# Optimization experiments

Hardware: AMD Instinct MI355X
Metric: run time of the kernel (lower is better)

## Reference

```python
import jax, jax.numpy as jnp
import numpy as np

T, B, I, H, L, O = 512, 64, 128, 512, 2, 256


def _lstm_layer(x, Wih, Whh, b):
    """One LSTM layer over time. x:[T,B,in] -> (ys:[T,B,H], hT:[B,H], cT:[B,H]).
    PyTorch gate order: i, f, g, o. Zero initial state (module's zero buffers)."""
    Hs = Whh.shape[1]
    # Precompute input contribution for all timesteps (one big GEMM).
    xg = jnp.einsum('tbi,gi->tbg', x, Wih) + b  # [T,B,4H]

    def step(carry, xt):
        h, c = carry
        g = xt + h @ Whh.T  # [B,4H]
        i, f, gg, o = jnp.split(g, 4, axis=-1)
        c = jax.nn.sigmoid(f) * c + jax.nn.sigmoid(i) * jnp.tanh(gg)
        h = jax.nn.sigmoid(o) * jnp.tanh(c)
        return (h, c), h

    h0 = jnp.zeros((x.shape[1], Hs), x.dtype)
    (hT, cT), ys = jax.lax.scan(step, (h0, h0), xg)
    return ys, hT, cT


def setup_inputs() -> dict:
    key = jax.random.key(0)
    ks = jax.random.split(key, 9)
    s = 1.0 / np.sqrt(H)  # torch default uniform(-1/sqrt(H), 1/sqrt(H)) scale
    u = lambda k, shp: jax.random.uniform(k, shp, jnp.float32, -s, s)
    return {
        'x': jax.random.normal(ks[0], (T, B, I), jnp.float32),
        'W_ih0': u(ks[1], (4 * H, I)),
        'W_hh0': u(ks[2], (4 * H, H)),
        'b0': u(ks[3], (4 * H,)),  # b_ih + b_hh combined
        'W_ih1': u(ks[4], (4 * H, H)),
        'W_hh1': u(ks[5], (4 * H, H)),
        'b1': u(ks[6], (4 * H,)),
        'fc_w': u(ks[7], (O, H)),
        'fc_b': u(ks[8], (O,)),
    }


def reference(x, W_ih0, W_hh0, b0, W_ih1, W_hh1, b1, fc_w, fc_b):
    y0, h0, c0 = _lstm_layer(x, W_ih0, W_hh0, b0)
    y1, h1, c1 = _lstm_layer(y0, W_ih1, W_hh1, b1)
    fc = jnp.einsum('tbh,oh->tbo', y1, fc_w) + fc_b  # fused output projection
    hN = jnp.stack([h0, h1])  # [L,B,H]
    cN = jnp.stack([c0, c1])
    return fc, (hN, cN)
```

## Files before the change

kernel.cpp:

```cpp
#include <hip/hip_runtime.h>
#include <hip/hip_bf16.h>

#define T_SEQ 512
#define BATCH 64
#define IN0   128
#define HID   512
#define OUTF  256
#define G4    (4*HID)
#define NWG_L 64
#define FSTR  32

typedef __attribute__((ext_vector_type(8))) short short8;
typedef __attribute__((ext_vector_type(4))) float f32x4;
typedef unsigned short u16;
typedef unsigned long long u64;

__device__ __forceinline__ float sigmoidf_(float x) { return 1.f / (1.f + __expf(-x)); }
__device__ __forceinline__ float tanhf_(float x)    { return 1.f - 2.f / (1.f + __expf(2.f * x)); }

__device__ __forceinline__ u16 f2bf(float f) {
    union { float f; unsigned u; } a; a.f = f;
    unsigned u = a.u;
    return (u16)((u + 0x7fffu + ((u >> 16) & 1u)) >> 16);
}

__device__ __forceinline__ void wave_poll_ge(const unsigned* flags, int lane, unsigned tgt) {
    unsigned it = 0;
    for (;;) {
        unsigned v = __hip_atomic_load(flags + (size_t)lane * FSTR,
                                       __ATOMIC_RELAXED, __HIP_MEMORY_SCOPE_AGENT);
        if (__all((int)(v >= tgt))) return;
        __builtin_amdgcn_s_sleep(1);
        if ((++it & 2047u) == 0u)
            (void)__hip_atomic_load(flags, __ATOMIC_ACQUIRE, __HIP_MEMORY_SCOPE_AGENT);
    }
}

__global__ void cvt_f32_bf16(const float* __restrict__ in, u16* __restrict__ out, int n4) {
    int i = blockIdx.x * blockDim.x + threadIdx.x;
    if (i < n4) {
        float4 v = reinterpret_cast<const float4*>(in)[i];
        ushort4 o;
        o.x = f2bf(v.x); o.y = f2bf(v.y); o.z = f2bf(v.z); o.w = f2bf(v.w);
        reinterpret_cast<ushort4*>(out)[i] = o;
    }
}

template<int LAYER>
__device__ __forceinline__ void run_layer(
    const u16* __restrict__ asrc,
    const u16* __restrict__ wih, const u16* __restrict__ whh,
    const float* __restrict__ bias,
    u16* __restrict__ ybuf,
    float* __restrict__ hNout, float* __restrict__ cNout,
    unsigned* flags_own, unsigned* flags_dep, int g,
    u16 (*lds_w)[32][512], float (*lds_g)[33], float (*lds_b)[16],
    unsigned (*lds_h)[4])
{
    constexpr int KIN = (LAYER == 0) ? IN0 : HID;
    constexpr int KS1 = KIN / 32;
    constexpr int KS  = KS1 + 16;

    const int tid  = threadIdx.x;
    const int lane = tid & 63;
    const int w    = tid >> 6;
    const int ubase = 8 * g;

    for (int idx = tid; idx < 2 * KS * 64; idx += 256) {
        int nt  = (idx >= KS * 64) ? 1 : 0;
        int rem = idx - nt * KS * 64;
        int ks = rem >> 6, s = rem & 63, q = s & 15, kq = s >> 4;
        int r = (q >> 2) * HID + ubase + 4 * nt + (q & 3);
        const u16* src = (ks < KS1)
            ? wih + (size_t)r * KIN + (size_t)ks * 32 + kq * 8
            : whh + (size_t)r * HID + (size_t)(ks - KS1) * 32 + kq * 8;
        *reinterpret_cast<uint4*>(&lds_w[nt][ks][s * 8]) =
            *reinterpret_cast<const uint4*>(src);
    }
    if (tid < 32) {
        int nt = tid >> 4, q = tid & 15;
        lds_b[nt][q] = bias[(q >> 2) * HID + ubase + 4 * nt + (q & 3)];
    }
    __syncthreads();

    const int pb  = tid & 63;
    const int pu2 = tid >> 6;
    float c0 = 0.f, c1 = 0.f;

    const int arow = 16 * w + (lane & 15);
    const int koff = (lane >> 4) * 8;

    for (int t = 0; t < T_SEQ; ++t) {
        f32x4 ac0[4] = {{0,0,0,0},{0,0,0,0},{0,0,0,0},{0,0,0,0}};
        f32x4 ac1[4] = {{0,0,0,0},{0,0,0,0},{0,0,0,0},{0,0,0,0}};

        if (LAYER == 0) {
            const u16* ap = asrc + ((size_t)t * BATCH + arow) * KIN + koff;
            short8 a[KS1];
            #pragma unroll
            for (int j = 0; j < KS1; ++j)
                a[j] = *reinterpret_cast<const short8*>(ap + j * 32);
            #pragma unroll
            for (int j = 0; j < KS1; ++j) {
                ac0[j & 3] = __builtin_amdgcn_mfma_f32_16x16x32_bf16(
                    a[j], *reinterpret_cast<const short8*>(&lds_w[0][j][lane * 8]), ac0[j & 3], 0, 0, 0);
                ac1[j & 3] = __builtin_amdgcn_mfma_f32_16x16x32_bf16(
                    a[j], *reinterpret_cast<const short8*>(&lds_w[1][j][lane * 8]), ac1[j & 3], 0, 0, 0);
            }
        }

        if (LAYER == 0) {
            if (t > 0) {
                if (w == 0) wave_poll_ge(flags_own, lane, (unsigned)t);
                __syncthreads();
            }
        } else {
            if (w == 0 && t > 0) wave_poll_ge(flags_own, lane, (unsigned)t);
            if (w == 1) wave_poll_ge(flags_dep, lane, (unsigned)(t + 1));
            __syncthreads();
        }

        if (t > 0) {
            const u16* hp = ybuf + ((size_t)(t - 1) * BATCH + arow) * HID + koff;
            short8 a[16];
            #pragma unroll
            for (int j = 0; j < 16; ++j)
                a[j] = *reinterpret_cast<const short8*>(hp + j * 32);
            #pragma unroll
            for (int j = 0; j < 16; ++j) {
                ac0[j & 3] = __builtin_amdgcn_mfma_f32_16x16x32_bf16(
                    a[j], *reinterpret_cast<const short8*>(&lds_w[0][KS1 + j][lane * 8]), ac0[j & 3], 0, 0, 0);
                ac1[j & 3] = __builtin_amdgcn_mfma_f32_16x16x32_bf16(
                    a[j], *reinterpret_cast<const short8*>(&lds_w[1][KS1 + j][lane * 8]), ac1[j & 3], 0, 0, 0);
            }
        }

        if (LAYER == 1) {
            const u16* ap = asrc + ((size_t)t * BATCH + arow) * HID + koff;
            short8 a[16];
            #pragma unroll
            for (int j = 0; j < 16; ++j)
                a[j] = *reinterpret_cast<const short8*>(ap + j * 32);
            #pragma unroll
            for (int j = 0; j < 16; ++j) {
                ac0[j & 3] = __builtin_amdgcn_mfma_f32_16x16x32_bf16(
                    a[j], *reinterpret_cast<const short8*>(&lds_w[0][j][lane * 8]), ac0[j & 3], 0, 0, 0);
                ac1[j & 3] = __builtin_amdgcn_mfma_f32_16x16x32_bf16(
                    a[j], *reinterpret_cast<const short8*>(&lds_w[1][j][lane * 8]), ac1[j & 3], 0, 0, 0);
            }
        }

        f32x4 s0 = (ac0[0] + ac0[1]) + (ac0[2] + ac0[3]);
        f32x4 s1 = (ac1[0] + ac1[1]) + (ac1[2] + ac1[3]);
        #pragma unroll
        for (int j = 0; j < 4; ++j) {
            int row = 16 * w + (lane >> 4) * 4 + j;
            lds_g[row][lane & 15]        = s0[j];
            lds_g[row][16 + (lane & 15)] = s1[j];
        }
        __syncthreads();

        {
            const int nt = pu2 >> 1;
            const int dq = (2 * pu2) & 3;
            const float* gr = &lds_g[pb][nt * 16];
            const float* br = lds_b[nt];
            float gi0 = sigmoidf_(gr[dq]      + br[dq]);
            float gf0 = sigmoidf_(gr[4 + dq]  + br[4 + dq]);
            float gg0 = tanhf_(   gr[8 + dq]  + br[8 + dq]);
            float go0 = sigmoidf_(gr[12 + dq] + br[12 + dq]);
            c0 = gf0 * c0 + gi0 * gg0;
            float h0v = go0 * tanhf_(c0);
            float gi1 = sigmoidf_(gr[dq + 1]      + br[dq + 1]);
            float gf1 = sigmoidf_(gr[4 + dq + 1]  + br[4 + dq + 1]);
            float gg1 = tanhf_(   gr[8 + dq + 1]  + br[8 + dq + 1]);
            float go1 = sigmoidf_(gr[12 + dq + 1] + br[12 + dq + 1]);
            c1 = gf1 * c1 + gi1 * gg1;
            float h1v = go1 * tanhf_(c1);

            lds_h[pb][pu2] = (unsigned)f2bf(h0v) | ((unsigned)f2bf(h1v) << 16);

            if (t == T_SEQ - 1) {
                hNout[pb * HID + ubase + 2 * pu2]     = h0v;
                hNout[pb * HID + ubase + 2 * pu2 + 1] = h1v;
                cNout[pb * HID + ubase + 2 * pu2]     = c0;
                cNout[pb * HID + ubase + 2 * pu2 + 1] = c1;
            }
        }
        __syncthreads();

        if (w == 0) {
            uint4 hv = *reinterpret_cast<const uint4*>(&lds_h[lane][0]);
            u64 q0 = (u64)hv.x | ((u64)hv.y << 32);
            u64 q1 = (u64)hv.z | ((u64)hv.w << 32);
            u64* yp = reinterpret_cast<u64*>(
                ybuf + ((size_t)t * BATCH + lane) * HID + ubase);
            __hip_atomic_store(yp + 0, q0, __ATOMIC_RELAXED, __HIP_MEMORY_SCOPE_AGENT);
            __hip_atomic_store(yp + 1, q1, __ATOMIC_RELAXED, __HIP_MEMORY_SCOPE_AGENT);
            asm volatile("s_waitcnt vmcnt(0)" ::: "memory");
            if (lane == 0)
                __hip_atomic_store(flags_own + (size_t)g * FSTR, (unsigned)(t + 1),
                                   __ATOMIC_RELAXED, __HIP_MEMORY_SCOPE_AGENT);
        }
    }
}

__global__ __launch_bounds__(256, 1)
void lstm_fused(const u16* __restrict__ x_bf,
                const u16* __restrict__ wih0, const u16* __restrict__ whh0, const float* __restrict__ b0,
                const u16* __restrict__ wih1, const u16* __restrict__ whh1, const float* __restrict__ b1,
                u16* __restrict__ y0, u16* __restrict__ y1,
                float* __restrict__ hN, float* __restrict__ cN,
                unsigned* __restrict__ ctr)
{
    __shared__ __align__(16) u16 lds_w[2][32][512];
    __shared__ float lds_g[BATCH][33];
    __shared__ float lds_b[2][16];
    __shared__ __align__(16) unsigned lds_h[BATCH][4];

    unsigned* flags0 = ctr;
    unsigned* flags1 = ctr + NWG_L * FSTR;

    const int wgid = blockIdx.x;
    if (wgid < NWG_L) {
        run_layer<0>(x_bf, wih0, whh0, b0, y0, hN, cN,
                     flags0, flags0, wgid, lds_w, lds_g, lds_b, lds_h);
    } else {
        run_layer<1>(y0, wih1, whh1, b1, y1, hN + BATCH * HID, cN + BATCH * HID,
                     flags1, flags0, wgid - NWG_L, lds_w, lds_g, lds_b, lds_h);
    }
}

__global__ __launch_bounds__(256)
void fc_kernel(const u16* __restrict__ y1, const u16* __restrict__ fcw,
               const float* __restrict__ fcb, float* __restrict__ out)
{
    const int tid  = threadIdx.x;
    const int lane = tid & 63;
    const int wgid = blockIdx.x * 4 + (tid >> 6);
    const int nq   = wgid & 3;
    const int mt0  = wgid >> 2;

    for (int j = 0; j < 8; ++j) {
        int mt = mt0 + j * 256;
        f32x4 acc[4] = {{0,0,0,0},{0,0,0,0},{0,0,0,0},{0,0,0,0}};
        const u16* arow = y1 + ((size_t)mt * 16 + (lane & 15)) * HID + (lane >> 4) * 8;
        #pragma unroll
        for (int ks = 0; ks < 16; ++ks) {
            short8 a = *reinterpret_cast<const short8*>(arow + ks * 32);
            #pragma unroll
            for (int nt = 0; nt < 4; ++nt) {
                const u16* brow = fcw + ((size_t)(nq * 64 + nt * 16 + (lane & 15))) * HID
                                      + ks * 32 + (lane >> 4) * 8;
                short8 b = *reinterpret_cast<const short8*>(brow);
                acc[nt] = __builtin_amdgcn_mfma_f32_16x16x32_bf16(a, b, acc[nt], 0, 0, 0);
            }
        }
        #pragma unroll
        for (int nt = 0; nt < 4; ++nt) {
            int col = nq * 64 + nt * 16 + (lane & 15);
            float bb = fcb[col];
            #pragma unroll
            for (int jj = 0; jj < 4; ++jj) {
                int row = mt * 16 + (lane >> 4) * 4 + jj;
                out[(size_t)row * OUTF + col] = acc[nt][jj] + bb;
            }
        }
    }
}

extern "C" void kernel_launch(void* const* d_in, const int* in_sizes, int n_in,
                              void* d_out, int out_size, void* d_ws, size_t ws_size,
                              hipStream_t stream)
{
    const float* x    = (const float*)d_in[0];
    const float* wih0 = (const float*)d_in[1];
    const float* whh0 = (const float*)d_in[2];
    const float* b0   = (const float*)d_in[3];
    const float* wih1 = (const float*)d_in[4];
    const float* whh1 = (const float*)d_in[5];
    const float* b1   = (const float*)d_in[6];
    const float* fcw  = (const float*)d_in[7];
    const float* fcb  = (const float*)d_in[8];
    float* out = (float*)d_out;

    const size_t flag_bytes = (size_t)2 * NWG_L * FSTR * 4;

    char* ws = (char*)d_ws;
    size_t off = 0;
    unsigned* ctr = (unsigned*)ws;                    off += flag_bytes;
    u16* x_bf    = (u16*)(ws + off);                  off += (size_t)T_SEQ * BATCH * IN0 * 2;
    u16* wih0_bf = (u16*)(ws + off);                  off += (size_t)G4 * IN0 * 2;
    u16* whh0_bf = (u16*)(ws + off);                  off += (size_t)G4 * HID * 2;
    u16* wih1_bf = (u16*)(ws + off);                  off += (size_t)G4 * HID * 2;
    u16* whh1_bf = (u16*)(ws + off);                  off += (size_t)G4 * HID * 2;
    u16* fcw_bf  = (u16*)(ws + off);                  off += (size_t)OUTF * HID * 2;
    u16* y0      = (u16*)(ws + off);                  off += (size_t)T_SEQ * BATCH * HID * 2;
    u16* y1      = (u16*)(ws + off);                  off += (size_t)T_SEQ * BATCH * HID * 2;

    hipMemsetAsync(ctr, 0, flag_bytes, stream);

    auto conv = [&](const float* in, u16* o, int n) {
        int n4 = n / 4;
        cvt_f32_bf16<<<(n4 + 255) / 256, 256, 0, stream>>>(in, o, n4);
    };
    conv(x,    x_bf,    T_SEQ * BATCH * IN0);
    conv(wih0, wih0_bf, G4 * IN0);
    conv(whh0, whh0_bf, G4 * HID);
    conv(wih1, wih1_bf, G4 * HID);
    conv(whh1, whh1_bf, G4 * HID);
    conv(fcw,  fcw_bf,  OUTF * HID);

    float* outFC = out;
    float* hN = out + (size_t)T_SEQ * BATCH * OUTF;
    float* cN = hN + 2 * BATCH * HID;

    lstm_fused<<<2 * NWG_L, 256, 0, stream>>>(x_bf, wih0_bf, whh0_bf, b0,
                                              wih1_bf, whh1_bf, b1,
                                              y0, y1, hN, cN, ctr);
    fc_kernel<<<256, 256, 0, stream>>>(y1, fcw_bf, fcb, outFC);
}
```

Measured before the change: 3.498 ms.

## Poll producer flags per k-group and interleave with MFMA, drop block barrier

The block-wide barrier after polling all producer flags is replaced by per-wave polling of 16-flag groups. After each group is ready, the wave immediately issues the MFMAs for the matching k-slices, for both the recurrent and the layer-1 input contributions. The goal is to overlap waiting on late producers with the math on chunks that are already available, and to remove a __syncthreads per step. The cost is more flag traffic, since every wave now polls, and fewer loads in flight at a time. The final hN/cN store indexing is also corrected to match the unit mapping used in the gate computation.

New measurement: 3.360 ms. 1.04x faster.

```diff
diff --git a/kernel.cpp b/kernel.cpp
--- a/kernel.cpp
+++ b/kernel.cpp
@@ -24,15 +24,15 @@
     return (u16)((u + 0x7fffu + ((u >> 16) & 1u)) >> 16);
 }
 
-__device__ __forceinline__ void wave_poll_ge(const unsigned* flags, int lane, unsigned tgt) {
+__device__ __forceinline__ void poll_grp(const unsigned* flags, int lane, int grp, unsigned tgt) {
+    const unsigned* p = flags + (size_t)(grp * 16 + (lane & 15)) * FSTR;
     unsigned it = 0;
     for (;;) {
-        unsigned v = __hip_atomic_load(flags + (size_t)lane * FSTR,
-                                       __ATOMIC_RELAXED, __HIP_MEMORY_SCOPE_AGENT);
+        unsigned v = __hip_atomic_load(p, __ATOMIC_RELAXED, __HIP_MEMORY_SCOPE_AGENT);
         if (__all((int)(v >= tgt))) return;
         __builtin_amdgcn_s_sleep(1);
         if ((++it & 2047u) == 0u)
-            (void)__hip_atomic_load(flags, __ATOMIC_ACQUIRE, __HIP_MEMORY_SCOPE_AGENT);
+            (void)__hip_atomic_load(p, __ATOMIC_ACQUIRE, __HIP_MEMORY_SCOPE_AGENT);
     }
 }
 
@@ -107,46 +107,35 @@
                 ac1[j & 3] = __builtin_amdgcn_mfma_f32_16x16x32_bf16(
                     a[j], *reinterpret_cast<const short8*>(&lds_w[1][j][lane * 8]), ac1[j & 3], 0, 0, 0);
             }
-        }
-
-        if (LAYER == 0) {
-            if (t > 0) {
-                if (w == 0) wave_poll_ge(flags_own, lane, (unsigned)t);
-                __syncthreads();
-            }
         } else {
-            if (w == 0 && t > 0) wave_poll_ge(flags_own, lane, (unsigned)t);
-            if (w == 1) wave_poll_ge(flags_dep, lane, (unsigned)(t + 1));
-            __syncthreads();
+            const u16* ap = asrc + ((size_t)t * BATCH + arow) * HID + koff;
+            for (int grp = 0; grp < 4; ++grp) {
+                poll_grp(flags_dep, lane, grp, (unsigned)(t + 1));
+                #pragma unroll
+                for (int j = 0; j < 4; ++j) {
+                    int ks = grp * 4 + j;
+                    short8 a = *reinterpret_cast<const short8*>(ap + ks * 32);
+                    ac0[j] = __builtin_amdgcn_mfma_f32_16x16x32_bf16(
+                        a, *reinterpret_cast<const short8*>(&lds_w[0][ks][lane * 8]), ac0[j], 0, 0, 0);
+                    ac1[j] = __builtin_amdgcn_mfma_f32_16x16x32_bf16(
+                        a, *reinterpret_cast<const short8*>(&lds_w[1][ks][lane * 8]), ac1[j], 0, 0, 0);
+                }
+            }
         }
 
         if (t > 0) {
             const u16* hp = ybuf + ((size_t)(t - 1) * BATCH + arow) * HID + koff;
-            short8 a[16];
-            #pragma unroll
-            for (int j = 0; j < 16; ++j)
-                a[j] = *reinterpret_cast<const short8*>(hp + j * 32);
-            #pragma unroll
-            for (int j = 0; j < 16; ++j) {
-                ac0[j & 3] = __builtin_amdgcn_mfma_f32_16x16x32_bf16(
-                    a[j], *reinterpret_cast<const short8*>(&lds_w[0][KS1 + j][lane * 8]), ac0[j & 3], 0, 0, 0);
-                ac1[j & 3] = __builtin_amdgcn_mfma_f32_16x16x32_bf16(
-                    a[j], *reinterpret_cast<const short8*>(&lds_w[1][KS1 + j][lane * 8]), ac1[j & 3], 0, 0, 0);
-            }
-        }
-
-        if (LAYER == 1) {
-            const u16* ap = asrc + ((size_t)t * BATCH + arow) * HID + koff;
-            short8 a[16];
-            #pragma unroll
-            for (int j = 0; j < 16; ++j)
-                a[j] = *reinterpret_cast<const short8*>(ap + j * 32);
-            #pragma unroll
-            for (int j = 0; j < 16; ++j) {
-                ac0[j & 3] = __builtin_amdgcn_mfma_f32_16x16x32_bf16(
-                    a[j], *reinterpret_cast<const short8*>(&lds_w[0][j][lane * 8]), ac0[j & 3], 0, 0, 0);
-                ac1[j & 3] = __builtin_amdgcn_mfma_f32_16x16x32_bf16(
-                    a[j], *reinterpret_cast<const short8*>(&lds_w[1][j][lane * 8]), ac1[j & 3], 0, 0, 0);
+            for (int grp = 0; grp < 4; ++grp) {
+                poll_grp(flags_own, lane, grp, (unsigned)t);
+                #pragma unroll
+                for (int j = 0; j < 4; ++j) {
+                    int ks = grp * 4 + j;
+                    short8 a = *reinterpret_cast<const short8*>(hp + ks * 32);
+                    ac0[j] = __builtin_amdgcn_mfma_f32_16x16x32_bf16(
+                        a, *reinterpret_cast<const short8*>(&lds_w[0][KS1 + ks][lane * 8]), ac0[j], 0, 0, 0);
+                    ac1[j] = __builtin_amdgcn_mfma_f32_16x16x32_bf16(
+                        a, *reinterpret_cast<const short8*>(&lds_w[1][KS1 + ks][lane * 8]), ac1[j], 0, 0, 0);
+                }
             }
         }
 
@@ -181,10 +170,11 @@
             lds_h[pb][pu2] = (unsigned)f2bf(h0v) | ((unsigned)f2bf(h1v) << 16);
 
             if (t == T_SEQ - 1) {
-                hNout[pb * HID + ubase + 2 * pu2]     = h0v;
-                hNout[pb * HID + ubase + 2 * pu2 + 1] = h1v;
-                cNout[pb * HID + ubase + 2 * pu2]     = c0;
-                cNout[pb * HID + ubase + 2 * pu2 + 1] = c1;
+                const int u0 = ubase + 4 * nt + dq, u1 = u0 + 1;
+                hNout[pb * HID + u0] = h0v;
+                hNout[pb * HID + u1] = h1v;
+                cNout[pb * HID + u0] = c0;
+                cNout[pb * HID + u1] = c1;
             }
         }
         __syncthreads();
```
